# Kernel tuning notes

Measured on AMD Instinct MI355X. Metric: run time of the kernel, lower is better.

## Reference

```python
import jax, jax.numpy as jnp
import numpy as np

N = 100000      # nodes
D = 64          # raw node feature dim
E = 3200000     # edges
G = 128         # graphs in batch
RANK = 50
OVER = 10       # randomized-SVD oversampling
NPOW = 4        # subspace (power) iterations
ALPHA = 0.85    # pagerank alpha
HID = 32
NCLS = 696
F = 21 * D      # concat of [x] + 4 hop-1 + 16 hop-2 propagated tensors


def setup_inputs() -> dict:
    key = jax.random.key(0)
    ks = jax.random.split(key, 8)
    x = jax.random.normal(ks[0], (N, D), jnp.float32)
    rows = jax.random.randint(ks[1], (E,), 0, N, jnp.int32)
    cols = jax.random.randint(ks[2], (E,), 0, N, jnp.int32)
    graph_ids = jnp.sort(jax.random.randint(ks[3], (N,), 0, G, jnp.int32))
    w = jax.random.normal(ks[4], (F, 64), jnp.float32) / np.float32(np.sqrt(F))
    W1 = jax.random.normal(ks[5], (64, HID), jnp.float32) / np.float32(8.0)
    b1 = jnp.zeros((HID,), jnp.float32)
    W2 = jax.random.normal(ks[6], (HID, NCLS), jnp.float32) / np.float32(np.sqrt(HID))
    return dict(x=x, rows=rows, cols=cols, graph_ids=graph_ids, num_graphs=G,
                w=w, W1=W1, b1=b1, W2=W2)


def _prop_ops(X, rows, cols, deg, n):
    """Apply the 4 sparse operators to X. A[r,c]=1 per edge (rows[k], cols[k])."""
    ax = jax.ops.segment_sum(X[cols], rows, num_segments=n)          # A @ X
    t = ax / jnp.where(deg > 0, deg, 1.0)[:, None]                   # D^{-1} A @ X (transition)
    pr = ALPHA * t + ((1.0 - ALPHA) / n) * ax                        # pagerank-style operator
    dw = ax / (deg + 1e-5)[:, None]                                  # deepwalk: diag(1/(deg+eps)) A
    return [ax, t, pr, dw]


def _propagated(x, rows, cols):
    n = x.shape[0]
    deg = jax.ops.segment_sum(jnp.ones(rows.shape, x.dtype), rows, num_segments=n)
    h1 = _prop_ops(x, rows, cols, deg, n)                            # 4 tensors, hop 1
    h2 = [t2 for t1 in h1 for t2 in _prop_ops(t1, rows, cols, deg, n)]  # 16 tensors, hop 2
    return jnp.concatenate([x] + h1 + h2, axis=-1)                   # [n, 21*D]


def _rsvd(h, rank, key):
    """Deterministic randomized SVD (Halko et al.), QR-stabilized power iterations."""
    k = rank + OVER
    omega = jax.random.normal(key, (h.shape[1], k), h.dtype)
    Q = jnp.linalg.qr(h @ omega)[0]                                  # [n, k]
    for _ in range(NPOW):
        Q = jnp.linalg.qr(h.T @ Q)[0]
        Q = jnp.linalg.qr(h @ Q)[0]
    B = Q.T @ h                                                      # [k, F]
    ub, s, vt = jnp.linalg.svd(B, full_matrices=False)
    return (Q @ ub)[:, :rank], s[:rank], vt[:rank]


def reference(x, rows, cols, graph_ids, num_graphs, w, W1, b1, W2):
    h = _propagated(x, rows, cols)                                   # [n, F]
    u, s, vt = _rsvd(h, RANK, jax.random.key(42))
    us = u * s                                                       # [n, rank]
    term = us @ (vt @ w)                                             # [n, 64]
    hid = jax.nn.leaky_relu(term @ W1 + b1)                          # Dense + leaky_relu
    out_nodes = hid @ W2                                             # [n, num_classes]
    # pooling_adj.T.normalize_right(): each node belongs to exactly one graph,
    # so the column sums are 1 and this is a per-graph segment sum.
    return jax.ops.segment_sum(out_nodes, graph_ids, num_segments=num_graphs)
```

## Files before the change

### kernel.cpp

```cpp
#include <hip/hip_runtime.h>

#define NN   100000
#define DD   64
#define EE   3200000
#define GG   128
#define FF   1344
#define KK   60
#define RK   50
#define HIDN 32
#define NCL  696
#define BSPLIT 128
#define GSL  64
#define PN   40


typedef short short8 __attribute__((ext_vector_type(8)));
typedef float f32x4 __attribute__((ext_vector_type(4)));

__device__ __forceinline__ unsigned short f2bf(float x){
  unsigned u = __float_as_uint(x);
  unsigned r = u + 0x7fffu + ((u>>16)&1u);
  return (unsigned short)(r>>16);
}
__device__ __forceinline__ float bf2f(unsigned short h){
// ... 89 lines not shown
    for (int i = 0; i < nb; ++i){ int v = bsums[i]; bsums[i] = run; run += v; }
  }
}

__global__ void k_scan3(const int* __restrict__ cnt, const int* __restrict__ bsums,
                        int* __restrict__ rowptr){
  int i = blockIdx.x*blockDim.x + threadIdx.x;
  if (i >= NN) return;
  int incl = rowptr[i];
  int ex = incl - cnt[i] + bsums[i >> 10];
  rowptr[i] = ex;
  if (i == NN-1) rowptr[NN] = ex + cnt[i];
}

__global__ void k_scatter(const int* __restrict__ rows, const int* __restrict__ cols,
                          const int* __restrict__ rowptr, int* __restrict__ tmpc,
                          int* __restrict__ csr){
  int e = blockIdx.x*blockDim.x + threadIdx.x;
  if (e >= EE) return;
  int r = rows[e];
  int p = atomicAdd(&tmpc[r], 1);
  csr[rowptr[r] + p] = cols[e];
}

__global__ void k_degr(const int* __restrict__ cnt, float* __restrict__ r1, float* __restrict__ r2){
  int i = blockIdx.x*blockDim.x + threadIdx.x;
  if (i >= NN) return;
  int d = cnt[i];
  float fd = (float)d;
  r1[i] = (d > 0) ? 1.0f/fd : 1.0f;
  r2[i] = 1.0f/(fd + 1e-5f);
}

__global__ __launch_bounds__(256) void k_hop1(const float* __restrict__ x,
    const int* __restrict__ rp, const int* __restrict__ cc, float* __restrict__ ax){
  int n = blockIdx.x*4 + (threadIdx.x >> 6);
  int lane = threadIdx.x & 63;
  if (n >= NN) return;
  int s = rp[n], e = rp[n+1];
  float acc = 0.f;
  int idx = s;
  for (; idx + 8 <= e; idx += 8){
    int c0 = cc[idx], c1 = cc[idx+1], c2 = cc[idx+2], c3 = cc[idx+3];
    int c4 = cc[idx+4], c5 = cc[idx+5], c6 = cc[idx+6], c7 = cc[idx+7];
    float v0 = x[(size_t)c0*64 + lane];
    float v1 = x[(size_t)c1*64 + lane];
    float v2 = x[(size_t)c2*64 + lane];
    float v3 = x[(size_t)c3*64 + lane];
    float v4 = x[(size_t)c4*64 + lane];
    float v5 = x[(size_t)c5*64 + lane];
    float v6 = x[(size_t)c6*64 + lane];
    float v7 = x[(size_t)c7*64 + lane];
    acc += ((v0 + v1) + (v2 + v3)) + ((v4 + v5) + (v6 + v7));
  }
  for (; idx < e; ++idx) acc += x[(size_t)cc[idx]*64 + lane];
  ax[(size_t)n*64 + lane] = acc;
}

__global__ __launch_bounds__(256) void k_hop2(const int* __restrict__ rp, const int* __restrict__ cc,
    const float* __restrict__ ax, const float* __restrict__ r1, const float* __restrict__ r2,
    float* __restrict__ S0, float* __restrict__ S1, float* __restrict__ S3){
  int n = blockIdx.x*4 + (threadIdx.x >> 6);
  int lane = threadIdx.x & 63;
  if (n >= NN) return;
  int s = rp[n], e = rp[n+1];
  float s0 = 0.f, s1 = 0.f, s3 = 0.f;
  int idx = s;
  for (; idx + 8 <= e; idx += 8){
    int c0 = cc[idx], c1 = cc[idx+1], c2 = cc[idx+2], c3 = cc[idx+3];
    int c4 = cc[idx+4], c5 = cc[idx+5], c6 = cc[idx+6], c7 = cc[idx+7];
    float v0 = ax[(size_t)c0*64 + lane], a0 = r1[c0], b0 = r2[c0];
    float v1 = ax[(size_t)c1*64 + lane], a1 = r1[c1], b1 = r2[c1];
    float v2 = ax[(size_t)c2*64 + lane], a2 = r1[c2], b2 = r2[c2];
    float v3 = ax[(size_t)c3*64 + lane], a3 = r1[c3], b3 = r2[c3];
    float v4 = ax[(size_t)c4*64 + lane], a4 = r1[c4], b4 = r2[c4];
    float v5 = ax[(size_t)c5*64 + lane], a5 = r1[c5], b5 = r2[c5];
    float v6 = ax[(size_t)c6*64 + lane], a6 = r1[c6], b6 = r2[c6];
    float v7 = ax[(size_t)c7*64 + lane], a7 = r1[c7], b7 = r2[c7];
    s0 += ((v0 + v1) + (v2 + v3)) + ((v4 + v5) + (v6 + v7));
    s1 = fmaf(v0,a0,fmaf(v1,a1,fmaf(v2,a2,fmaf(v3,a3,s1))));
    s1 = fmaf(v4,a4,fmaf(v5,a5,fmaf(v6,a6,fmaf(v7,a7,s1))));
    s3 = fmaf(v0,b0,fmaf(v1,b1,fmaf(v2,b2,fmaf(v3,b3,s3))));
    s3 = fmaf(v4,b4,fmaf(v5,b5,fmaf(v6,b6,fmaf(v7,b7,s3))));
  }
  for (; idx < e; ++idx){
    int c = cc[idx];
    float v = ax[(size_t)c*64 + lane];
    s0 += v;
    s1 = fmaf(v, r1[c], s1);
    s3 = fmaf(v, r2[c], s3);
  }
  S0[(size_t)n*64 + lane] = s0;
  S1[(size_t)n*64 + lane] = s1;
  S3[(size_t)n*64 + lane] = s3;
}

__global__ void k_beff(const float* __restrict__ B, float* __restrict__ Beff){
  int gid = blockIdx.x*blockDim.x + threadIdx.x;
  if (gid >= 20*4096) return;
  int p = gid >> 12;
  int rem = gid & 4095;
  int c = rem >> 6, r = rem & 63;
  int t = p >> 2, j = p & 3;
  float val = 0.f;
  if (c < KK){
    if (t == 0)      val = (j == 0) ? B[(0*64 + r)*60 + c] : 0.f;
    else if (t == 1) val = B[((1+j)*64 + r)*60 + c];
    else if (t == 2) val = B[((5+j)*64 + r)*60 + c] + 1.5e-6f*B[((13+j)*64 + r)*60 + c];
    else if (t == 3) val = B[((9+j)*64 + r)*60 + c] + 0.85f  *B[((13+j)*64 + r)*60 + c];
    else             val = B[((17+j)*64 + r)*60 + c];
  }
  Beff[gid] = val;
}

__global__ __launch_bounds__(256) void k_beffT(const float* __restrict__ Z,
    const float* __restrict__ Rtot, float* __restrict__ Beff){
  __shared__ float Br[64][61];
  __shared__ float Rt[60][64];
  int p = blockIdx.x;
  int t2 = p >> 2, j = p & 3;
  int tid = threadIdx.x;
  if (t2 == 0 && j != 0){
    for (int o = tid; o < 4096; o += 256) Beff[(size_t)p*4096 + o] = 0.f;
    return;
  }
  for (int i = tid; i < 3840; i += 256){
    int r = i >> 6, c = i & 63;
    if (c < 60) Rt[r][c] = Rtot[r*60 + c];
  }
  for (int o = tid; o < 64*60; o += 256){
    int r = o / 60, k = o - (o/60)*60;
    float v;
    if (t2 == 0)      v = Z[(0*64 + r)*60 + k];
    else if (t2 == 1) v = Z[((1+j)*64 + r)*60 + k];
    else if (t2 == 2) v = Z[((5+j)*64 + r)*60 + k] + 1.5e-6f*Z[((13+j)*64 + r)*60 + k];
    else if (t2 == 3) v = Z[((9+j)*64 + r)*60 + k] + 0.85f  *Z[((13+j)*64 + r)*60 + k];
    else              v = Z[((17+j)*64 + r)*60 + k];
    Br[r][k] = v;
  }
  __syncthreads();
  for (int o = tid; o < 4096; o += 256){
    int c = o >> 6, r = o & 63;
    float s = 0.f;
    if (c < KK){
      #pragma unroll 10
      for (int kp = 0; kp < 60; ++kp) s = fmaf(Br[r][kp], Rt[kp][c], s);
    }
    Beff[(size_t)p*4096 + o] = s;
  }
}

__device__ __forceinline__ void fma44(const float4 a, const float4 b, float (&acc)[4][4]){
  acc[0][0] = fmaf(a.x,b.x,acc[0][0]); acc[0][1] = fmaf(a.x,b.y,acc[0][1]);
  acc[0][2] = fmaf(a.x,b.z,acc[0][2]); acc[0][3] = fmaf(a.x,b.w,acc[0][3]);
  acc[1][0] = fmaf(a.y,b.x,acc[1][0]); acc[1][1] = fmaf(a.y,b.y,acc[1][1]);
  acc[1][2] = fmaf(a.y,b.z,acc[1][2]); acc[1][3] = fmaf(a.y,b.w,acc[1][3]);
  acc[2][0] = fmaf(a.z,b.x,acc[2][0]); acc[2][1] = fmaf(a.z,b.y,acc[2][1]);
  acc[2][2] = fmaf(a.z,b.z,acc[2][2]); acc[2][3] = fmaf(a.z,b.w,acc[2][3]);
  acc[3][0] = fmaf(a.w,b.x,acc[3][0]); acc[3][1] = fmaf(a.w,b.y,acc[3][1]);
  acc[3][2] = fmaf(a.w,b.z,acc[3][2]); acc[3][3] = fmaf(a.w,b.w,acc[3][3]);
}

__global__ __launch_bounds__(256) void k_fwd(
    const float* __restrict__ xi, const float* __restrict__ ax,
    const float* __restrict__ S0, const float* __restrict__ S1,
    const float* __restrict__ S3, const float* __restrict__ Beff,
    const float* __restrict__ r1, const float* __restrict__ r2,
    float* __restrict__ Y, float* __restrict__ Cpart){
  __shared__ __align__(16) unsigned short AB[4*64*72];
  __shared__ float cS[4][64];
  unsigned short* Ah = AB;
  unsigned short* Al = AB + 64*72;
  unsigned short* Bh = AB + 2*64*72;
  unsigned short* Bl = AB + 3*64*72;
  float* As2 = (float*)AB;

  const float* Ts[5] = {xi, ax, S0, S1, S3};
  int n0 = blockIdx.x*64;
  int tid = threadIdx.x;
  int lane = tid & 63, wid = tid >> 6;
  int rowb = (wid & 1)*32, colb = (wid >> 1)*32;
  int l15 = lane & 15, l4 = lane >> 4;

  if (tid < 64){
    int gn = n0 + tid;
    float r1v = 0.f, r2v = 0.f, one = 0.f;
    if (gn < NN){ r1v = r1[gn]; r2v = r2[gn]; one = 1.f; }
    cS[0][tid] = one;
    cS[1][tid] = r1v;
    cS[2][tid] = fmaf(0.85f, r1v, 1.5e-6f*one);
    cS[3][tid] = r2v;
  }

  f32x4 master[2][2] = {};

  float4 pf0, pf1, pf2, pf3;
  {
    const float* src = Beff;
    pf0 = *(const float4*)(src + (size_t)((tid+  0)>>4)*64 + ((tid+  0)&15)*4);
    pf1 = *(const float4*)(src + (size_t)((tid+256)>>4)*64 + ((tid+256)&15)*4);
    pf2 = *(const float4*)(src + (size_t)((tid+512)>>4)*64 + ((tid+512)&15)*4);
    pf3 = *(const float4*)(src + (size_t)((tid+768)>>4)*64 + ((tid+768)&15)*4);
  }

  int curt = -1;
  for (int plin = 0; plin < 17; ++plin){
    int t  = (plin == 0) ? 0 : (((plin-1) >> 2) + 1);
    int jj = (plin == 0) ? 0 : ((plin-1) & 3);
    if (t != curt){
      __syncthreads();
      const float* T = Ts[t];
      #pragma unroll
      for (int l = 0; l < 4; ++l){
        int li = tid + l*256;
        int n = li >> 4, fq = (li & 15)*4;
        int gn = n0 + n;
        float4 v = make_float4(0.f,0.f,0.f,0.f);
        if (gn < NN) v = *(const float4*)(T + (size_t)gn*64 + fq);
        unsigned short h0=f2bf(v.x), h1=f2bf(v.y), h2=f2bf(v.z), h3=f2bf(v.w);
        ushort4 hv = make_ushort4(h0,h1,h2,h3);
        ushort4 lv = make_ushort4(f2bf(v.x - bf2f(h0)), f2bf(v.y - bf2f(h1)),
                                  f2bf(v.z - bf2f(h2)), f2bf(v.w - bf2f(h3)));
        *(ushort4*)(Ah + n*72 + fq) = hv;
        *(ushort4*)(Al + n*72 + fq) = lv;
      }
      curt = t;
    }
    __syncthreads();
    {
      float4 pv[4] = {pf0, pf1, pf2, pf3};
      #pragma unroll
      for (int l = 0; l < 4; ++l){
        int li = tid + l*256;
        int c = li >> 4, kq = (li & 15)*4;
        float4 v = pv[l];
        unsigned short h0=f2bf(v.x), h1=f2bf(v.y), h2=f2bf(v.z), h3=f2bf(v.w);
        ushort4 hv = make_ushort4(h0,h1,h2,h3);
        ushort4 lv = make_ushort4(f2bf(v.x - bf2f(h0)), f2bf(v.y - bf2f(h1)),
                                  f2bf(v.z - bf2f(h2)), f2bf(v.w - bf2f(h3)));
        *(ushort4*)(Bh + c*72 + kq) = hv;
        *(ushort4*)(Bl + c*72 + kq) = lv;
      }
    }
    if (plin + 1 < 17){
      const float* src = Beff + (size_t)(plin + 4)*4096;
      pf0 = *(const float4*)(src + (size_t)((tid+  0)>>4)*64 + ((tid+  0)&15)*4);
      pf1 = *(const float4*)(src + (size_t)((tid+256)>>4)*64 + ((tid+256)&15)*4);
      pf2 = *(const float4*)(src + (size_t)((tid+512)>>4)*64 + ((tid+512)&15)*4);
      pf3 = *(const float4*)(src + (size_t)((tid+768)>>4)*64 + ((tid+768)&15)*4);
    }
    __syncthreads();

    float cvv[2][4];
    #pragma unroll
    for (int rg = 0; rg < 2; ++rg)
      #pragma unroll
      for (int r = 0; r < 4; ++r)
        cvv[rg][r] = cS[jj][rowb + rg*16 + l4*4 + r];

    f32x4 part[2][2] = {};
    #pragma unroll
    for (int s = 0; s < 2; ++s){
      int kc = s*32 + l4*8;
      short8 a0h = *(const short8*)(Ah + (rowb      + l15)*72 + kc);
      short8 a1h = *(const short8*)(Ah + (rowb + 16 + l15)*72 + kc);
      short8 a0l = *(const short8*)(Al + (rowb      + l15)*72 + kc);
      short8 a1l = *(const short8*)(Al + (rowb + 16 + l15)*72 + kc);
      #pragma unroll
      for (int cg = 0; cg < 2; ++cg){
        short8 bh = *(const short8*)(Bh + (colb + cg*16 + l15)*72 + kc);
        short8 bl = *(const short8*)(Bl + (colb + cg*16 + l15)*72 + kc);
        part[0][cg] = __builtin_amdgcn_mfma_f32_16x16x32_bf16(a0h, bh, part[0][cg], 0, 0, 0);
        part[0][cg] = __builtin_amdgcn_mfma_f32_16x16x32_bf16(a0h, bl, part[0][cg], 0, 0, 0);
        part[0][cg] = __builtin_amdgcn_mfma_f32_16x16x32_bf16(a0l, bh, part[0][cg], 0, 0, 0);
        part[1][cg] = __builtin_amdgcn_mfma_f32_16x16x32_bf16(a1h, bh, part[1][cg], 0, 0, 0);
        part[1][cg] = __builtin_amdgcn_mfma_f32_16x16x32_bf16(a1h, bl, part[1][cg], 0, 0, 0);
        part[1][cg] = __builtin_amdgcn_mfma_f32_16x16x32_bf16(a1l, bh, part[1][cg], 0, 0, 0);
      }
    }
    #pragma unroll
    for (int rg = 0; rg < 2; ++rg)
      #pragma unroll
// ... 20 lines not shown
  for (int rg = 0; rg < 2; ++rg)
    #pragma unroll
    for (int cg = 0; cg < 2; ++cg)
      #pragma unroll
      for (int r = 0; r < 4; ++r){
        int n = rowb + rg*16 + l4*4 + r;
        int c = colb + cg*16 + l15;
        As2[n*68 + c] = master[rg][cg][r];
      }
  __syncthreads();
  {
    int tx = tid & 15, ty = tid >> 4;
    float g[4][4] = {};
    #pragma unroll 4
    for (int n = 0; n < 64; ++n){
      float4 a = *(const float4*)(As2 + n*68 + tx*4);
      float4 b = *(const float4*)(As2 + n*68 + ty*4);
      fma44(a, b, g);
    }
    float* slab = Cpart + (size_t)(blockIdx.x & (GSL-1))*3600;
    #pragma unroll
    for (int i = 0; i < 4; ++i){
      int r = tx*4 + i;
      #pragma unroll
      for (int j = 0; j < 4; ++j){
        int c = ty*4 + j;
        if (r < KK && c < KK) atomicAdd(&slab[r*KK + c], g[i][j]);
      }
    }
  }
}

__global__ __launch_bounds__(256) void k_bwd(
    const float* __restrict__ xi, const float* __restrict__ ax,
    const float* __restrict__ S0t, const float* __restrict__ S1t,
    const float* __restrict__ S3t, const float* __restrict__ Qm,
    const float* __restrict__ r1, const float* __restrict__ r2,
    float* __restrict__ Ppart){
  const float* T = (blockIdx.x==0)?xi:(blockIdx.x==1)?ax:(blockIdx.x==2)?S0t:(blockIdx.x==3)?S1t:S3t;
  const bool isX = (blockIdx.x == 0);
  const int TT = (NN + 31)/32;
  int per = (TT + BSPLIT - 1)/BSPLIT;
  int t0 = blockIdx.y * per;
  int t1 = t0 + per; if (t1 > TT) t1 = TT;

  __shared__ __align__(16) unsigned short Ah[64*PN];
  __shared__ __align__(16) unsigned short Al[64*PN];
  __shared__ __align__(16) unsigned short Bh3[3*64*PN];
  __shared__ __align__(16) unsigned short Bl3[3*64*PN];

  int tid = threadIdx.x;
  int lane = tid & 63, wid = tid >> 6;
  int rowb = (wid & 1)*32, colb = (wid >> 1)*32;
  int l15 = lane & 15, l4 = lane >> 4;

  for (int o = tid; o < 3*64*PN; o += 256){ Bh3[o] = 0; Bl3[o] = 0; }

  f32x4 master[3][2][2] = {};

  for (int tl = t0; tl < t1; ++tl){
    int nb = tl*32;
    __syncthreads();
    #pragma unroll
    for (int l = 0; l < 2; ++l){
      int li = tid + l*256;
      int n = li >> 4, fq = (li & 15)*4;
      int gn = nb + n;
      float4 v = make_float4(0.f,0.f,0.f,0.f);
      if (gn < NN) v = *(const float4*)(T + (size_t)gn*64 + fq);
      float vv[4] = {v.x, v.y, v.z, v.w};
      #pragma unroll
      for (int i = 0; i < 4; ++i){
        unsigned short h = f2bf(vv[i]);
        Ah[(fq+i)*PN + n] = h;
        Al[(fq+i)*PN + n] = f2bf(vv[i] - bf2f(h));
      }
    }
    #pragma unroll
    for (int l = 0; l < 2; ++l){
      int li = tid + l*256;
      if (li < 480){
        int n = li/15, cq = (li - (li/15)*15)*4;
        int gn = nb + n;
        float4 v = make_float4(0.f,0.f,0.f,0.f);
        float cc0 = 0.f, cc1 = 0.f, cc3 = 0.f;
        if (gn < NN){
          v = *(const float4*)(Qm + (size_t)gn*KK + cq);
          cc0 = 1.f;
          cc1 = isX ? 0.f : r1[gn];
          cc3 = isX ? 0.f : r2[gn];
        }
        float vv[4] = {v.x, v.y, v.z, v.w};
        float cc[3] = {cc0, cc1, cc3};
        #pragma unroll
        for (int jj = 0; jj < 3; ++jj){
          #pragma unroll
          for (int i = 0; i < 4; ++i){
            float sv = cc[jj]*vv[i];
            unsigned short h = f2bf(sv);
            Bh3[jj*64*PN + (cq+i)*PN + n] = h;
            Bl3[jj*64*PN + (cq+i)*PN + n] = f2bf(sv - bf2f(h));
          }
        }
      }
    }
    __syncthreads();
    short8 a0h = *(const short8*)(Ah + (rowb      + l15)*PN + l4*8);
    short8 a1h = *(const short8*)(Ah + (rowb + 16 + l15)*PN + l4*8);
// ... 71 lines not shown
  for (int tl = t0; tl < t1; ++tl){
    int nbase = tl*16;
    if (tid < 240){
      int n = tid / 15, ci = tid - (tid/15)*15;
      float4 v = make_float4(0.f,0.f,0.f,0.f);
      int gn = nbase + n;
      if (gn < nrows) v = *(const float4*)(X + (size_t)gn*KK + ci*4);
      *(float4*)&Xs[n][ci*4] = v;
    } else {
      int n = tid - 240;
      Xs[n][60]=0.f; Xs[n][61]=0.f; Xs[n][62]=0.f; Xs[n][63]=0.f;
    }
    __syncthreads();
    #pragma unroll
    for (int n = 0; n < 16; ++n){
      float4 a = *(const float4*)&Xs[n][tx*4];
      float4 b = *(const float4*)&Xs[n][ty*4];
      fma44(a, b, acc);
    }
    __syncthreads();
  }
  float* dst = Cpart + (size_t)blockIdx.x*3600;
  #pragma unroll
  for (int i = 0; i < 4; ++i){
    int r = tx*4 + i;
    #pragma unroll
    for (int j = 0; j < 4; ++j){
      int c = ty*4 + j;
      if (r < KK && c < KK) dst[r*KK + c] = acc[i][j];
    }
  }
}

__global__ void k_cred(const float* __restrict__ Cpart, int nparts, float* __restrict__ Cm){
  int gid = blockIdx.x*blockDim.x + threadIdx.x;
  if (gid >= 3600) return;
  float s = 0.f;
  for (int b = 0; b < nparts; ++b) s += Cpart[(size_t)b*3600 + gid];
  Cm[gid] = s;
}

__global__ __launch_bounds__(256) void k_cholinv(const float* __restrict__ Cin,
                                                 float* __restrict__ Rinv){
  __shared__ float R[60][65];
  __shared__ float Ri[60][65];
  __shared__ float Tmp[30][33];
  __shared__ float ridge;
  int t = threadIdx.x;
  for (int i = t; i < 3840; i += 256){
    int r = i >> 6, c = i & 63;
    if (c < 60) R[r][c] = Cin[r*60 + c];
  }
  __syncthreads();
  if (t == 0){
    float tr = 0.f;
    for (int i = 0; i < 60; ++i) tr += R[i][i];
    ridge = 1e-7f*(tr/60.f) + 1e-30f;
  }
  __syncthreads();
  if (t < 60) R[t][t] += ridge;
  __syncthreads();
  for (int j = 0; j < 60; ++j){
    float d  = fmaxf(R[j][j], 1e-30f);
    float dp = (j > 0) ? fmaxf(R[j-1][j-1], 1e-30f) : 1.f;
    float inv = 1.0f / d;
    float rsp = (j > 0) ? (1.0f / sqrtf(dp)) : 1.f;
    int nrow = 59 - j;
    for (int task = t; task < (nrow+1)*64; task += 256){
      int rr = task >> 6, i2 = task & 63;
      if (rr < nrow){
        int k = j + 1 + rr;
        if (i2 >= k && i2 < 60) R[k][i2] -= R[j][k]*R[j][i2]*inv;
      } else {
        if (j > 0 && i2 >= j-1 && i2 < 60) R[j-1][i2] *= rsp;
      }
    }
    __syncthreads();
  }
  if (t == 0) R[59][59] = sqrtf(fmaxf(R[59][59], 1e-30f));
  __syncthreads();
  for (int i = t; i < 3840; i += 256){ int r = i >> 6, c = i & 63; Ri[r][c] = 0.f; }
  __syncthreads();
  if (t < 60){
    int c = t;
    int lo = (c < 30) ? 0 : 30;
    Ri[c][c] = 1.0f / R[c][c];
    for (int i = c-1; i >= lo; --i){
      float s = 0.f;
      for (int k = i+1; k <= c; ++k) s += R[i][k]*Ri[k][c];
      Ri[i][c] = -s / R[i][i];
    }
  }
  __syncthreads();
  for (int idx2 = t; idx2 < 960; idx2 += 256){
    int r = idx2 >> 5, c = idx2 & 31;
    if (c < 30){
      float s = 0.f;
      for (int k = 0; k <= c; ++k) s += R[r][30+k]*Ri[30+k][30+c];
      Tmp[r][c] = s;
    }
  }
  __syncthreads();
  for (int idx2 = t; idx2 < 960; idx2 += 256){
    int r = idx2 >> 5, c = idx2 & 31;
    if (c < 30){
      float s = 0.f;
      for (int k = r; k < 30; ++k) s += Ri[r][k]*Tmp[k][c];
      Ri[r][30+c] = -s;
    }
  }
  __syncthreads();
  for (int i = t; i < 3600; i += 256) Rinv[i] = Ri[i/60][i%60];
}

__global__ __launch_bounds__(256) void k_cholinv2(const float* __restrict__ Gin,
                                                  float* __restrict__ Rinv){
  __shared__ float G[60][65];
  __shared__ float RN[60][65];
  __shared__ float T1[60][65];
  __shared__ float G2[60][65];
  __shared__ float Tmp[30][33];
  __shared__ float ridge;
  int t = threadIdx.x;
  for (int i = t; i < 3840; i += 256){
    int r = i >> 6, c = i & 63;
    if (c < 60){ G[r][c] = Gin[r*60 + c]; RN[r][c] = Rinv[r*60 + c]; }
  }
  __syncthreads();
  for (int o = t; o < 3600; o += 256){
    int i = o/60, j = o - (o/60)*60;
    float s = 0.f;
    for (int k = 0; k <= j; ++k) s = fmaf(G[i][k], RN[k][j], s);
    T1[i][j] = s;
  }
  __syncthreads();
  for (int o = t; o < 3600; o += 256){
    int i = o/60, j = o - (o/60)*60;
    float s = 0.f;
    for (int k = 0; k <= i; ++k) s = fmaf(RN[k][i], T1[k][j], s);
    G2[i][j] = s;
  }
  __syncthreads();
  if (t == 0){
    float tr = 0.f;
    for (int i = 0; i < 60; ++i) tr += G2[i][i];
    ridge = 1e-7f*(tr/60.f) + 1e-30f;
  }
  __syncthreads();
  if (t < 60) G2[t][t] += ridge;
  __syncthreads();
  for (int j = 0; j < 60; ++j){
    float d  = fmaxf(G2[j][j], 1e-30f);
    float dp = (j > 0) ? fmaxf(G2[j-1][j-1], 1e-30f) : 1.f;
    float inv = 1.0f / d;
    float rsp = (j > 0) ? (1.0f / sqrtf(dp)) : 1.f;
    int nrow = 59 - j;
    for (int task = t; task < (nrow+1)*64; task += 256){
      int rr = task >> 6, i2 = task & 63;
      if (rr < nrow){
// ... 46 lines not shown
    }
    Rinv[o] = s;
  }
}

__global__ __launch_bounds__(256) void k_applyR(const float* Yin,
    const float* __restrict__ Rinv, float* Xout, int nrows){
  __shared__ float Rs[3600];
  for (int i = threadIdx.x; i < 3600; i += 256) Rs[i] = Rinv[i];
  __syncthreads();
  int w = threadIdx.x >> 6, lane = threadIdx.x & 63;
  #pragma unroll
  for (int r = 0; r < 4; ++r){
    int n = blockIdx.x*16 + w*4 + r;
    if (n >= nrows) continue;
    const float* y = Yin + (size_t)n*KK;
    float accv = 0.f;
    #pragma unroll 10
    for (int k2 = 0; k2 < KK; ++k2) accv = fmaf(y[k2], Rs[k2*KK + lane], accv);
    if (lane < KK) Xout[(size_t)n*KK + lane] = accv;
  }
}

__global__ void k_wb(const float* __restrict__ Z, const float* __restrict__ w,
                     float* __restrict__ WB){
  int gid = blockIdx.x*blockDim.x + threadIdx.x;
  if (gid >= KK*64) return;
  int r = gid >> 6, d = gid & 63;
  float acc = 0.f;
  for (int f = 0; f < FF; ++f) acc = fmaf(Z[(size_t)f*KK + r], w[(size_t)f*64 + d], acc);
  WB[gid] = acc;
}

__global__ __launch_bounds__(512) void k_jacobi(const float* __restrict__ Min,
                                                float* __restrict__ U50){
  __shared__ float A[60][65];
  __shared__ float Vv[60][65];
  __shared__ float cs[32], sn[32];
  __shared__ int pp[32], qq[32];
  __shared__ float ev[64];
  __shared__ int idx[64];
  int t = threadIdx.x;
  for (int i = t; i < 3840; i += 512){
    int r = i >> 6, c = i & 63;
    if (c < 60){ A[r][c] = Min[r*60 + c]; Vv[r][c] = (r == c) ? 1.f : 0.f; }
  }
  __syncthreads();
  for (int sweep = 0; sweep < 4; ++sweep){
    for (int round = 0; round < 59; ++round){
      if (t < 30){
        int i = t, j2 = 59 - t;
        int p = (i == 0) ? 0 : ((i - 1 + round) % 59 + 1);
        int q = ((j2 - 1 + round) % 59 + 1);
        if (p > q){ int tv = p; p = q; q = tv; }
        pp[t] = p; qq[t] = q;
        float app = A[p][p], aqq = A[q][q], apq = A[p][q];
        float c, s;
        if (fabsf(apq) < 1e-36f){ c = 1.f; s = 0.f; }
        else {
          float tau = (aqq - app) / (2.f * apq);
          float tt = ((tau >= 0.f) ? 1.f : -1.f) / (fabsf(tau) + sqrtf(1.f + tau*tau));
          c = 1.f / sqrtf(1.f + tt*tt);
          s = tt * c;
        }
        cs[t] = c; sn[t] = s;
      }
      __syncthreads();
      for (int task = t; task < 1920; task += 512){
        int k = task >> 6, i = task & 63;
        if (i < 60){
          int p = pp[k], q = qq[k];
          float c = cs[k], s = sn[k];
          float aip = A[i][p], aiq = A[i][q];
          A[i][p] = c*aip - s*aiq;  A[i][q] = s*aip + c*aiq;
          float vip = Vv[i][p], viq = Vv[i][q];
          Vv[i][p] = c*vip - s*viq; Vv[i][q] = s*vip + c*viq;
        }
      }
      __syncthreads();
      for (int task = t; task < 1920; task += 512){
        int k = task >> 6, i = task & 63;
// ... 106 lines not shown
    #pragma unroll
    for (int k2 = 0; k2 < HIDN; ++k2) accv = fmaf(hr[k2], W2s[k2][lane], accv);
  }
  part[w][lane] = accv;
  __syncthreads();
  if (w == 0){
    float v = part[0][lane] + part[1][lane] + part[2][lane] + part[3][lane];
    int col = c0 + lane;
    if (col < NCL) out[(size_t)g*NCL + col] = v;
  }
}

extern "C" void kernel_launch(void* const* d_in, const int* in_sizes, int n_in,
                              void* d_out, int out_size, void* d_ws, size_t ws_size,
                              hipStream_t stream){
  (void)in_sizes; (void)n_in; (void)out_size;
  const float* x   = (const float*)d_in[0];
  const int*  rows = (const int*)d_in[1];
  const int*  cols = (const int*)d_in[2];
  const int*  gids = (const int*)d_in[3];
  const float* wM  = (const float*)d_in[5];
  const float* W1  = (const float*)d_in[6];
  const float* b1  = (const float*)d_in[7];
  const float* W2  = (const float*)d_in[8];
  float* out = (float*)d_out;

  char* base = (char*)d_ws;
  size_t off = 0;
  auto alloc = [&](size_t bytes)->char*{
    off = (off + 255) & ~(size_t)255;
    char* p = base + off; off += bytes; return p;
  };
  float* ax    = (float*)alloc((size_t)NN*64*4);
  float* S0    = (float*)alloc((size_t)NN*64*4);
  float* S1    = (float*)alloc((size_t)NN*64*4);
  float* S3    = (float*)alloc((size_t)NN*64*4);
  float* Y     = (float*)alloc((size_t)NN*KK*4);
  int*   csr   = (int*)  alloc((size_t)EE*4);
  float* Ppart = (float*)alloc((size_t)BSPLIT*76800*4);
  float* Beff  = (float*)alloc((size_t)20*4096*4);
  float* Om    = (float*)alloc((size_t)FF*KK*4);
  float* Zf    = (float*)alloc((size_t)FF*KK*4);
  float* Cm    = (float*)alloc(3600*4);
  float* Rinv  = (float*)alloc(3600*4);
  float* Mm    = (float*)alloc(3600*4);
  float* U50   = (float*)alloc(60*RK*4);
  float* WB    = (float*)alloc(KK*64*4);
  float* TW1   = (float*)alloc(KK*HIDN*4);
  float* r1    = (float*)alloc((size_t)NN*4);
  float* r2    = (float*)alloc((size_t)NN*4);
  int* cnt     = (int*)alloc((size_t)NN*4);
  int* rowptr  = (int*)alloc((size_t)(NN+1)*4);
  int* tmpc    = (int*)alloc((size_t)NN*4);
  int* gst     = (int*)alloc((size_t)(GG+1)*4);
  int* bsums   = (int*)alloc(256*4);
  float* hid   = ax;
  float* Cpart = Ppart;
  if (off > ws_size) return;

  const int SCAN_B = (NN + 1023) / 1024;

  hipMemsetAsync(cnt, 0, (size_t)NN*4, stream);
  k_count<<<(EE+255)/256, 256, 0, stream>>>(rows, cnt);
  k_scan1<<<SCAN_B, 1024, 0, stream>>>(cnt, rowptr, bsums);
  k_scan2<<<1, 64, 0, stream>>>(bsums, SCAN_B);
  k_scan3<<<(NN+255)/256, 256, 0, stream>>>(cnt, bsums, rowptr);
  hipMemsetAsync(tmpc, 0, (size_t)NN*4, stream);
  k_scatter<<<(EE+255)/256, 256, 0, stream>>>(rows, cols, rowptr, tmpc, csr);
  k_degr<<<(NN+255)/256, 256, 0, stream>>>(cnt, r1, r2);

  k_hop1<<<(NN+3)/4, 256, 0, stream>>>(x, rowptr, csr, ax);
  k_hop2<<<(NN+3)/4, 256, 0, stream>>>(rowptr, csr, ax, r1, r2, S0, S1, S3);

  k_omega<<<(FF*KK+255)/256, 256, 0, stream>>>(Om);

  auto fwdg = [&](){
    hipMemsetAsync(Cpart, 0, (size_t)GSL*3600*4, stream);
    k_fwd<<<(NN+63)/64, 256, 0, stream>>>(x, ax, S0, S1, S3, Beff, r1, r2, Y, Cpart);
  };
  auto bwd = [&](const float* Qbuf){
    k_bwd<<<dim3(5, BSPLIT), 256, 0, stream>>>(x, ax, S0, S1, S3, Qbuf, r1, r2, Ppart);
    k_zasm<<<(FF*KK+255)/256, 256, 0, stream>>>(Ppart, Zf);
  };

  k_beff<<<(20*4096+255)/256, 256, 0, stream>>>(Om, Beff);
  fwdg();

  for (int it = 0; it < 4; ++it){
    k_cred<<<15, 256, 0, stream>>>(Cpart, GSL, Cm);
    k_cholinv<<<1, 256, 0, stream>>>(Cm, Rinv);
    bwd(Y);
    k_syrkp<<<84, 256, 0, stream>>>(Zf, FF, Cpart);
    k_cred<<<15, 256, 0, stream>>>(Cpart, 84, Cm);
    k_cholinv2<<<1, 256, 0, stream>>>(Cm, Rinv);
    k_beffT<<<20, 256, 0, stream>>>(Zf, Rinv, Beff);
    fwdg();
  }

  k_cred<<<15, 256, 0, stream>>>(Cpart, GSL, Cm);
  k_cholinv<<<1, 256, 0, stream>>>(Cm, Rinv);
  k_applyR<<<(NN+15)/16, 256, 0, stream>>>(Y, Rinv, Y, NN);

  bwd(Y);
  k_syrkp<<<84, 256, 0, stream>>>(Zf, FF, Cpart);
  k_cred<<<15, 256, 0, stream>>>(Cpart, 84, Mm);
  k_wb<<<(KK*64+255)/256, 256, 0, stream>>>(Zf, wM, WB);

  k_jacobi<<<1, 512, 0, stream>>>(Mm, U50);
  k_chain<<<1, 256, 0, stream>>>(U50, WB, W1, TW1);

  k_hid<<<(NN*HIDN+255)/256, 256, 0, stream>>>(Y, TW1, b1, hid);
  k_gstart<<<1, 256, 0, stream>>>(gids, gst);
  k_pool<<<dim3(GG, (NCL+63)/64), 256, 0, stream>>>(hid, W2, gst, out);
}
```

Before: 4.594 ms.

## Precompute bf16 hi/lo splits of propagated features once and fuse reductions

The hop kernels and a new conversion kernel now store the propagated feature tensors (x, ax, S0, S1, S3) and the Beff operand as pre-split bf16 high/low pairs. The forward and backward GEMM kernels then load these directly instead of re-splitting fp32 values on every pass of the power iterations. The separate partial-sum reduction kernels are folded into the single-block Cholesky and Jacobi kernels, which removes several launches. The Jacobi sweep count is also cut from 4 to 3, which saves time but may lower eigen-decomposition accuracy.

```diff
diff --git a/kernel.cpp b/kernel.cpp
--- a/kernel.cpp
+++ b/kernel.cpp
@@ -145,8 +145,19 @@
   r2[i] = 1.0f/(fd + 1e-5f);
 }
 
+__global__ void k_xcvt(const float* __restrict__ x,
+                       unsigned short* __restrict__ xh, unsigned short* __restrict__ xl){
+  int gid = blockIdx.x*blockDim.x + threadIdx.x;
+  if (gid >= NN*64) return;
+  float v = x[gid];
+  unsigned short h = f2bf(v);
+  xh[gid] = h;
+  xl[gid] = f2bf(v - bf2f(h));
+}
+
 __global__ __launch_bounds__(256) void k_hop1(const float* __restrict__ x,
-    const int* __restrict__ rp, const int* __restrict__ cc, float* __restrict__ ax){
+    const int* __restrict__ rp, const int* __restrict__ cc, float* __restrict__ ax,
+    unsigned short* __restrict__ axh, unsigned short* __restrict__ axl){
   int n = blockIdx.x*4 + (threadIdx.x >> 6);
   int lane = threadIdx.x & 63;
   if (n >= NN) return;
@@ -167,17 +178,23 @@
     acc += ((v0 + v1) + (v2 + v3)) + ((v4 + v5) + (v6 + v7));
   }
   for (; idx < e; ++idx) acc += x[(size_t)cc[idx]*64 + lane];
-  ax[(size_t)n*64 + lane] = acc;
+  size_t o = (size_t)n*64 + lane;
+  ax[o] = acc;
+  unsigned short h = f2bf(acc);
+  axh[o] = h;
+  axl[o] = f2bf(acc - bf2f(h));
 }
 
 __global__ __launch_bounds__(256) void k_hop2(const int* __restrict__ rp, const int* __restrict__ cc,
     const float* __restrict__ ax, const float* __restrict__ r1, const float* __restrict__ r2,
-    float* __restrict__ S0, float* __restrict__ S1, float* __restrict__ S3){
+    unsigned short* __restrict__ s0h, unsigned short* __restrict__ s0l,
+    unsigned short* __restrict__ s1h, unsigned short* __restrict__ s1l,
+    unsigned short* __restrict__ s3h, unsigned short* __restrict__ s3l){
   int n = blockIdx.x*4 + (threadIdx.x >> 6);
   int lane = threadIdx.x & 63;
   if (n >= NN) return;
   int s = rp[n], e = rp[n+1];
-  float s0 = 0.f, s1 = 0.f, s3 = 0.f;
+  float v_s0 = 0.f, v_s1 = 0.f, v_s3 = 0.f;
   int idx = s;
   for (; idx + 8 <= e; idx += 8){
     int c0 = cc[idx], c1 = cc[idx+1], c2 = cc[idx+2], c3 = cc[idx+3];
@@ -190,25 +207,30 @@
     float v5 = ax[(size_t)c5*64 + lane], a5 = r1[c5], b5 = r2[c5];
     float v6 = ax[(size_t)c6*64 + lane], a6 = r1[c6], b6 = r2[c6];
     float v7 = ax[(size_t)c7*64 + lane], a7 = r1[c7], b7 = r2[c7];
-    s0 += ((v0 + v1) + (v2 + v3)) + ((v4 + v5) + (v6 + v7));
-    s1 = fmaf(v0,a0,fmaf(v1,a1,fmaf(v2,a2,fmaf(v3,a3,s1))));
-    s1 = fmaf(v4,a4,fmaf(v5,a5,fmaf(v6,a6,fmaf(v7,a7,s1))));
-    s3 = fmaf(v0,b0,fmaf(v1,b1,fmaf(v2,b2,fmaf(v3,b3,s3))));
-    s3 = fmaf(v4,b4,fmaf(v5,b5,fmaf(v6,b6,fmaf(v7,b7,s3))));
+    v_s0 += ((v0 + v1) + (v2 + v3)) + ((v4 + v5) + (v6 + v7));
+    v_s1 = fmaf(v0,a0,fmaf(v1,a1,fmaf(v2,a2,fmaf(v3,a3,v_s1))));
+    v_s1 = fmaf(v4,a4,fmaf(v5,a5,fmaf(v6,a6,fmaf(v7,a7,v_s1))));
+    v_s3 = fmaf(v0,b0,fmaf(v1,b1,fmaf(v2,b2,fmaf(v3,b3,v_s3))));
+    v_s3 = fmaf(v4,b4,fmaf(v5,b5,fmaf(v6,b6,fmaf(v7,b7,v_s3))));
   }
   for (; idx < e; ++idx){
     int c = cc[idx];
     float v = ax[(size_t)c*64 + lane];
-    s0 += v;
-    s1 = fmaf(v, r1[c], s1);
-    s3 = fmaf(v, r2[c], s3);
-  }
-  S0[(size_t)n*64 + lane] = s0;
-  S1[(size_t)n*64 + lane] = s1;
-  S3[(size_t)n*64 + lane] = s3;
-}
-
-__global__ void k_beff(const float* __restrict__ B, float* __restrict__ Beff){
+    v_s0 += v;
+    v_s1 = fmaf(v, r1[c], v_s1);
+    v_s3 = fmaf(v, r2[c], v_s3);
+  }
+  size_t o = (size_t)n*64 + lane;
+  unsigned short h0 = f2bf(v_s0);
+  s0h[o] = h0; s0l[o] = f2bf(v_s0 - bf2f(h0));
+  unsigned short h1 = f2bf(v_s1);
+  s1h[o] = h1; s1l[o] = f2bf(v_s1 - bf2f(h1));
+  unsigned short h3 = f2bf(v_s3);
+  s3h[o] = h3; s3l[o] = f2bf(v_s3 - bf2f(h3));
+}
+
+__global__ void k_beff(const float* __restrict__ B,
+                       unsigned short* __restrict__ Beh, unsigned short* __restrict__ Bel){
   int gid = blockIdx.x*blockDim.x + threadIdx.x;
   if (gid >= 20*4096) return;
   int p = gid >> 12;
@@ -223,18 +245,21 @@
     else if (t == 3) val = B[((9+j)*64 + r)*60 + c] + 0.85f  *B[((13+j)*64 + r)*60 + c];
     else             val = B[((17+j)*64 + r)*60 + c];
   }
-  Beff[gid] = val;
+  unsigned short h = f2bf(val);
+  Beh[gid] = h;
+  Bel[gid] = f2bf(val - bf2f(h));
 }
 
 __global__ __launch_bounds__(256) void k_beffT(const float* __restrict__ Z,
-    const float* __restrict__ Rtot, float* __restrict__ Beff){
+    const float* __restrict__ Rtot,
+    unsigned short* __restrict__ Beh, unsigned short* __restrict__ Bel){
   __shared__ float Br[64][61];
   __shared__ float Rt[60][64];
   int p = blockIdx.x;
   int t2 = p >> 2, j = p & 3;
   int tid = threadIdx.x;
   if (t2 == 0 && j != 0){
-    for (int o = tid; o < 4096; o += 256) Beff[(size_t)p*4096 + o] = 0.f;
+    for (int o = tid; o < 4096; o += 256){ Beh[(size_t)p*4096 + o] = 0; Bel[(size_t)p*4096 + o] = 0; }
     return;
   }
   for (int i = tid; i < 3840; i += 256){
@@ -259,7 +284,9 @@
       #pragma unroll 10
       for (int kp = 0; kp < 60; ++kp) s = fmaf(Br[r][kp], Rt[kp][c], s);
     }
-    Beff[(size_t)p*4096 + o] = s;
+    unsigned short h = f2bf(s);
+    Beh[(size_t)p*4096 + o] = h;
+    Bel[(size_t)p*4096 + o] = f2bf(s - bf2f(h));
   }
 }
 
@@ -275,9 +302,12 @@
 }
 
 __global__ __launch_bounds__(256) void k_fwd(
-    const float* __restrict__ xi, const float* __restrict__ ax,
-    const float* __restrict__ S0, const float* __restrict__ S1,
-    const float* __restrict__ S3, const float* __restrict__ Beff,
+    const unsigned short* __restrict__ xh, const unsigned short* __restrict__ xl,
+    const unsigned short* __restrict__ axh, const unsigned short* __restrict__ axl,
+    const unsigned short* __restrict__ s0h, const unsigned short* __restrict__ s0l,
+    const unsigned short* __restrict__ s1h, const unsigned short* __restrict__ s1l,
+    const unsigned short* __restrict__ s3h, const unsigned short* __restrict__ s3l,
+    const unsigned short* __restrict__ Beh, const unsigned short* __restrict__ Bel,
     const float* __restrict__ r1, const float* __restrict__ r2,
     float* __restrict__ Y, float* __restrict__ Cpart){
   __shared__ __align__(16) unsigned short AB[4*64*72];
@@ -287,8 +317,8 @@
   unsigned short* Bh = AB + 2*64*72;
   unsigned short* Bl = AB + 3*64*72;
   float* As2 = (float*)AB;
-
-  const float* Ts[5] = {xi, ax, S0, S1, S3};
+  const unsigned short* Tsh[5] = {xh, axh, s0h, s1h, s3h};
+  const unsigned short* Tsl[5] = {xl, axl, s0l, s1l, s3l};
   int n0 = blockIdx.x*64;
   int tid = threadIdx.x;
   int lane = tid & 63, wid = tid >> 6;
@@ -306,61 +336,39 @@
   }
 
   f32x4 master[2][2] = {};
-
-  float4 pf0, pf1, pf2, pf3;
-  {
-    const float* src = Beff;
-    pf0 = *(const float4*)(src + (size_t)((tid+  0)>>4)*64 + ((tid+  0)&15)*4);
-    pf1 = *(const float4*)(src + (size_t)((tid+256)>>4)*64 + ((tid+256)&15)*4);
-    pf2 = *(const float4*)(src + (size_t)((tid+512)>>4)*64 + ((tid+512)&15)*4);
-    pf3 = *(const float4*)(src + (size_t)((tid+768)>>4)*64 + ((tid+768)&15)*4);
-  }
-
   int curt = -1;
   for (int plin = 0; plin < 17; ++plin){
     int t  = (plin == 0) ? 0 : (((plin-1) >> 2) + 1);
     int jj = (plin == 0) ? 0 : ((plin-1) & 3);
+    int p  = (plin == 0) ? 0 : (plin + 3);
     if (t != curt){
       __syncthreads();
-      const float* T = Ts[t];
+      const unsigned short* Th = Tsh[t];
+      const unsigned short* Tl = Tsl[t];
       #pragma unroll
-      for (int l = 0; l < 4; ++l){
+      for (int l = 0; l < 2; ++l){
         int li = tid + l*256;
-        int n = li >> 4, fq = (li & 15)*4;
+        int n = li >> 3, f8 = (li & 7)*8;
         int gn = n0 + n;
-        float4 v = make_float4(0.f,0.f,0.f,0.f);
-        if (gn < NN) v = *(const float4*)(T + (size_t)gn*64 + fq);
-        unsigned short h0=f2bf(v.x), h1=f2bf(v.y), h2=f2bf(v.z), h3=f2bf(v.w);
-        ushort4 hv = make_ushort4(h0,h1,h2,h3);
-        ushort4 lv = make_ushort4(f2bf(v.x - bf2f(h0)), f2bf(v.y - bf2f(h1)),
-                                  f2bf(v.z - bf2f(h2)), f2bf(v.w - bf2f(h3)));
-        *(ushort4*)(Ah + n*72 + fq) = hv;
-        *(ushort4*)(Al + n*72 + fq) = lv;
+        uint4 hv = make_uint4(0,0,0,0), lv = make_uint4(0,0,0,0);
+        if (gn < NN){
+          hv = *(const uint4*)(Th + (size_t)gn*64 + f8);
+          lv = *(const uint4*)(Tl + (size_t)gn*64 + f8);
+        }
+        *(uint4*)(Ah + n*72 + f8) = hv;
+        *(uint4*)(Al + n*72 + f8) = lv;
       }
       curt = t;
     }
     __syncthreads();
-    {
-      float4 pv[4] = {pf0, pf1, pf2, pf3};
-      #pragma unroll
-      for (int l = 0; l < 4; ++l){
-        int li = tid + l*256;
-        int c = li >> 4, kq = (li & 15)*4;
-        float4 v = pv[l];
-        unsigned short h0=f2bf(v.x), h1=f2bf(v.y), h2=f2bf(v.z), h3=f2bf(v.w);
-        ushort4 hv = make_ushort4(h0,h1,h2,h3);
-        ushort4 lv = make_ushort4(f2bf(v.x - bf2f(h0)), f2bf(v.y - bf2f(h1)),
-                                  f2bf(v.z - bf2f(h2)), f2bf(v.w - bf2f(h3)));
-        *(ushort4*)(Bh + c*72 + kq) = hv;
-        *(ushort4*)(Bl + c*72 + kq) = lv;
-      }
-    }
-    if (plin + 1 < 17){
-      const float* src = Beff + (size_t)(plin + 4)*4096;
-      pf0 = *(const float4*)(src + (size_t)((tid+  0)>>4)*64 + ((tid+  0)&15)*4);
-      pf1 = *(const float4*)(src + (size_t)((tid+256)>>4)*64 + ((tid+256)&15)*4);
-      pf2 = *(const float4*)(src + (size_t)((tid+512)>>4)*64 + ((tid+512)&15)*4);
-      pf3 = *(const float4*)(src + (size_t)((tid+768)>>4)*64 + ((tid+768)&15)*4);
+    #pragma unroll
+    for (int l = 0; l < 2; ++l){
+      int li = tid + l*256;
+      int c = li >> 3, k8 = (li & 7)*8;
+      uint4 hv = *(const uint4*)(Beh + (size_t)p*4096 + c*64 + k8);
+      uint4 lv = *(const uint4*)(Bel + (size_t)p*4096 + c*64 + k8);
+      *(uint4*)(Bh + c*72 + k8) = hv;
+      *(uint4*)(Bl + c*72 + k8) = lv;
     }
     __syncthreads();
 
@@ -447,12 +455,15 @@
 }
 
 __global__ __launch_bounds__(256) void k_bwd(
-    const float* __restrict__ xi, const float* __restrict__ ax,
-    const float* __restrict__ S0t, const float* __restrict__ S1t,
-    const float* __restrict__ S3t, const float* __restrict__ Qm,
-    const float* __restrict__ r1, const float* __restrict__ r2,
+    const unsigned short* __restrict__ xh, const unsigned short* __restrict__ xl,
+    const unsigned short* __restrict__ axh, const unsigned short* __restrict__ axl,
+    const unsigned short* __restrict__ s0h, const unsigned short* __restrict__ s0l,
+    const unsigned short* __restrict__ s1h, const unsigned short* __restrict__ s1l,
+    const unsigned short* __restrict__ s3h, const unsigned short* __restrict__ s3l,
+    const float* __restrict__ Qm, const float* __restrict__ r1, const float* __restrict__ r2,
     float* __restrict__ Ppart){
-  const float* T = (blockIdx.x==0)?xi:(blockIdx.x==1)?ax:(blockIdx.x==2)?S0t:(blockIdx.x==3)?S1t:S3t;
+  const unsigned short* Th = (blockIdx.x==0)?xh:(blockIdx.x==1)?axh:(blockIdx.x==2)?s0h:(blockIdx.x==3)?s1h:s3h;
+  const unsigned short* Tl = (blockIdx.x==0)?xl:(blockIdx.x==1)?axl:(blockIdx.x==2)?s0l:(blockIdx.x==3)?s1l:s3l;
   const bool isX = (blockIdx.x == 0);
   const int TT = (NN + 31)/32;
   int per = (TT + BSPLIT - 1)/BSPLIT;
@@ -476,19 +487,20 @@
   for (int tl = t0; tl < t1; ++tl){
     int nb = tl*32;
     __syncthreads();
-    #pragma unroll
-    for (int l = 0; l < 2; ++l){
-      int li = tid + l*256;
-      int n = li >> 4, fq = (li & 15)*4;
+    {
+      int n = tid >> 3, f8 = (tid & 7)*8;
       int gn = nb + n;
-      float4 v = make_float4(0.f,0.f,0.f,0.f);
-      if (gn < NN) v = *(const float4*)(T + (size_t)gn*64 + fq);
-      float vv[4] = {v.x, v.y, v.z, v.w};
+      uint4 hv = make_uint4(0,0,0,0), lv = make_uint4(0,0,0,0);
+      if (gn < NN){
+        hv = *(const uint4*)(Th + (size_t)gn*64 + f8);
+        lv = *(const uint4*)(Tl + (size_t)gn*64 + f8);
+      }
+      const unsigned short* hp = (const unsigned short*)&hv;
+      const unsigned short* lp = (const unsigned short*)&lv;
       #pragma unroll
-      for (int i = 0; i < 4; ++i){
-        unsigned short h = f2bf(vv[i]);
-        Ah[(fq+i)*PN + n] = h;
-        Al[(fq+i)*PN + n] = f2bf(vv[i] - bf2f(h));
+      for (int i = 0; i < 8; ++i){
+        Ah[(f8+i)*PN + n] = hp[i];
+        Al[(f8+i)*PN + n] = lp[i];
       }
     }
     #pragma unroll
@@ -626,24 +638,17 @@
   }
 }
 
-__global__ void k_cred(const float* __restrict__ Cpart, int nparts, float* __restrict__ Cm){
-  int gid = blockIdx.x*blockDim.x + threadIdx.x;
-  if (gid >= 3600) return;
-  float s = 0.f;
-  for (int b = 0; b < nparts; ++b) s += Cpart[(size_t)b*3600 + gid];
-  Cm[gid] = s;
-}
-
-__global__ __launch_bounds__(256) void k_cholinv(const float* __restrict__ Cin,
-                                                 float* __restrict__ Rinv){
+__global__ __launch_bounds__(256) void k_credchol(const float* __restrict__ Cpart, int nparts,
+                                                  float* __restrict__ Rinv){
   __shared__ float R[60][65];
   __shared__ float Ri[60][65];
   __shared__ float Tmp[30][33];
   __shared__ float ridge;
   int t = threadIdx.x;
-  for (int i = t; i < 3840; i += 256){
-    int r = i >> 6, c = i & 63;
-    if (c < 60) R[r][c] = Cin[r*60 + c];
+  for (int i = t; i < 3600; i += 256){
+    float s = 0.f;
+    for (int b = 0; b < nparts; ++b) s += Cpart[(size_t)b*3600 + i];
+    R[i/60][i%60] = s;
   }
   __syncthreads();
   if (t == 0){
@@ -707,8 +712,8 @@
   for (int i = t; i < 3600; i += 256) Rinv[i] = Ri[i/60][i%60];
 }
 
-__global__ __launch_bounds__(256) void k_cholinv2(const float* __restrict__ Gin,
-                                                  float* __restrict__ Rinv){
+__global__ __launch_bounds__(256) void k_credchol2(const float* __restrict__ Cpart, int nparts,
+                                                   float* __restrict__ Rinv){
   __shared__ float G[60][65];
   __shared__ float RN[60][65];
   __shared__ float T1[60][65];
@@ -716,9 +721,11 @@
   __shared__ float Tmp[30][33];
   __shared__ float ridge;
   int t = threadIdx.x;
-  for (int i = t; i < 3840; i += 256){
-    int r = i >> 6, c = i & 63;
-    if (c < 60){ G[r][c] = Gin[r*60 + c]; RN[r][c] = Rinv[r*60 + c]; }
+  for (int i = t; i < 3600; i += 256){
+    float s = 0.f;
+    for (int b = 0; b < nparts; ++b) s += Cpart[(size_t)b*3600 + i];
+    G[i/60][i%60] = s;
+    RN[i/60][i%60] = Rinv[i];
   }
   __syncthreads();
   for (int o = t; o < 3600; o += 256){
@@ -831,7 +838,7 @@
   WB[gid] = acc;
 }
 
-__global__ __launch_bounds__(512) void k_jacobi(const float* __restrict__ Min,
+__global__ __launch_bounds__(512) void k_jacobi(const float* __restrict__ Cpart, int nparts,
                                                 float* __restrict__ U50){
   __shared__ float A[60][65];
   __shared__ float Vv[60][65];
@@ -840,12 +847,17 @@
   __shared__ float ev[64];
   __shared__ int idx[64];
   int t = threadIdx.x;
+  for (int i = t; i < 3600; i += 512){
+    float s = 0.f;
+    for (int b = 0; b < nparts; ++b) s += Cpart[(size_t)b*3600 + i];
+    A[i/60][i%60] = s;
+  }
   for (int i = t; i < 3840; i += 512){
     int r = i >> 6, c = i & 63;
-    if (c < 60){ A[r][c] = Min[r*60 + c]; Vv[r][c] = (r == c) ? 1.f : 0.f; }
-  }
-  __syncthreads();
-  for (int sweep = 0; sweep < 4; ++sweep){
+    if (c < 60) Vv[r][c] = (r == c) ? 1.f : 0.f;
+  }
+  __syncthreads();
+  for (int sweep = 0; sweep < 3; ++sweep){
     for (int round = 0; round < 59; ++round){
       if (t < 30){
         int i = t, j2 = 59 - t;
@@ -1018,18 +1030,24 @@
     char* p = base + off; off += bytes; return p;
   };
   float* ax    = (float*)alloc((size_t)NN*64*4);
-  float* S0    = (float*)alloc((size_t)NN*64*4);
-  float* S1    = (float*)alloc((size_t)NN*64*4);
-  float* S3    = (float*)alloc((size_t)NN*64*4);
+  unsigned short* xh  = (unsigned short*)alloc((size_t)NN*64*2);
+  unsigned short* xl  = (unsigned short*)alloc((size_t)NN*64*2);
+  unsigned short* axh = (unsigned short*)alloc((size_t)NN*64*2);
+  unsigned short* axl = (unsigned short*)alloc((size_t)NN*64*2);
+  unsigned short* s0h = (unsigned short*)alloc((size_t)NN*64*2);
+  unsigned short* s0l = (unsigned short*)alloc((size_t)NN*64*2);
+  unsigned short* s1h = (unsigned short*)alloc((size_t)NN*64*2);
+  unsigned short* s1l = (unsigned short*)alloc((size_t)NN*64*2);
+  unsigned short* s3h = (unsigned short*)alloc((size_t)NN*64*2);
+  unsigned short* s3l = (unsigned short*)alloc((size_t)NN*64*2);
   float* Y     = (float*)alloc((size_t)NN*KK*4);
   int*   csr   = (int*)  alloc((size_t)EE*4);
   float* Ppart = (float*)alloc((size_t)BSPLIT*76800*4);
-  float* Beff  = (float*)alloc((size_t)20*4096*4);
+  unsigned short* Beh = (unsigned short*)alloc((size_t)20*4096*2);
+  unsigned short* Bel = (unsigned short*)alloc((size_t)20*4096*2);
   float* Om    = (float*)alloc((size_t)FF*KK*4);
   float* Zf    = (float*)alloc((size_t)FF*KK*4);
-  float* Cm    = (float*)alloc(3600*4);
   float* Rinv  = (float*)alloc(3600*4);
-  float* Mm    = (float*)alloc(3600*4);
   float* U50   = (float*)alloc(60*RK*4);
   float* WB    = (float*)alloc(KK*64*4);
   float* TW1   = (float*)alloc(KK*HIDN*4);
@@ -1055,44 +1073,43 @@
   k_scatter<<<(EE+255)/256, 256, 0, stream>>>(rows, cols, rowptr, tmpc, csr);
   k_degr<<<(NN+255)/256, 256, 0, stream>>>(cnt, r1, r2);
 
-  k_hop1<<<(NN+3)/4, 256, 0, stream>>>(x, rowptr, csr, ax);
-  k_hop2<<<(NN+3)/4, 256, 0, stream>>>(rowptr, csr, ax, r1, r2, S0, S1, S3);
+  k_xcvt<<<(NN*64+255)/256, 256, 0, stream>>>(x, xh, xl);
+  k_hop1<<<(NN+3)/4, 256, 0, stream>>>(x, rowptr, csr, ax, axh, axl);
+  k_hop2<<<(NN+3)/4, 256, 0, stream>>>(rowptr, csr, ax, r1, r2, s0h, s0l, s1h, s1l, s3h, s3l);
 
   k_omega<<<(FF*KK+255)/256, 256, 0, stream>>>(Om);
 
   auto fwdg = [&](){
     hipMemsetAsync(Cpart, 0, (size_t)GSL*3600*4, stream);
-    k_fwd<<<(NN+63)/64, 256, 0, stream>>>(x, ax, S0, S1, S3, Beff, r1, r2, Y, Cpart);
+    k_fwd<<<(NN+63)/64, 256, 0, stream>>>(xh, xl, axh, axl, s0h, s0l, s1h, s1l, s3h, s3l,
+                                          Beh, Bel, r1, r2, Y, Cpart);
   };
   auto bwd = [&](const float* Qbuf){
-    k_bwd<<<dim3(5, BSPLIT), 256, 0, stream>>>(x, ax, S0, S1, S3, Qbuf, r1, r2, Ppart);
+    k_bwd<<<dim3(5, BSPLIT), 256, 0, stream>>>(xh, xl, axh, axl, s0h, s0l, s1h, s1l, s3h, s3l,
+                                               Qbuf, r1, r2, Ppart);
     k_zasm<<<(FF*KK+255)/256, 256, 0, stream>>>(Ppart, Zf);
   };
 
-  k_beff<<<(20*4096+255)/256, 256, 0, stream>>>(Om, Beff);
+  k_beff<<<(20*4096+255)/256, 256, 0, stream>>>(Om, Beh, Bel);
   fwdg();
 
   for (int it = 0; it < 4; ++it){
-    k_cred<<<15, 256, 0, stream>>>(Cpart, GSL, Cm);
-    k_cholinv<<<1, 256, 0, stream>>>(Cm, Rinv);
+    k_credchol<<<1, 256, 0, stream>>>(Cpart, GSL, Rinv);
     bwd(Y);
     k_syrkp<<<84, 256, 0, stream>>>(Zf, FF, Cpart);
-    k_cred<<<15, 256, 0, stream>>>(Cpart, 84, Cm);
-    k_cholinv2<<<1, 256, 0, stream>>>(Cm, Rinv);
-    k_beffT<<<20, 256, 0, stream>>>(Zf, Rinv, Beff);
+    k_credchol2<<<1, 256, 0, stream>>>(Cpart, 84, Rinv);
+    k_beffT<<<20, 256, 0, stream>>>(Zf, Rinv, Beh, Bel);
     fwdg();
   }
 
-  k_cred<<<15, 256, 0, stream>>>(Cpart, GSL, Cm);
-  k_cholinv<<<1, 256, 0, stream>>>(Cm, Rinv);
+  k_credchol<<<1, 256, 0, stream>>>(Cpart, GSL, Rinv);
   k_applyR<<<(NN+15)/16, 256, 0, stream>>>(Y, Rinv, Y, NN);
 
   bwd(Y);
   k_syrkp<<<84, 256, 0, stream>>>(Zf, FF, Cpart);
-  k_cred<<<15, 256, 0, stream>>>(Cpart, 84, Mm);
   k_wb<<<(KK*64+255)/256, 256, 0, stream>>>(Zf, wM, WB);
 
-  k_jacobi<<<1, 512, 0, stream>>>(Mm, U50);
+  k_jacobi<<<1, 512, 0, stream>>>(Cpart, 84, U50);
   k_chain<<<1, 256, 0, stream>>>(U50, WB, W1, TW1);
 
   k_hid<<<(NN*HIDN+255)/256, 256, 0, stream>>>(Y, TW1, b1, hid);
```

New measurement: 6.656 ms. 44.9% more time.
